# Optimization experiments

Measured on AMD Instinct MI355X. Metric: run time of the kernel, lower is better.

The kernel has to match this reference:

```python
import jax, jax.numpy as jnp
import numpy as np

BS, C, D = 4096, 16384, 128
POS_ALPHA, POS_DELTA = 32.0, 0.1
NEG_ALPHA, NEG_DELTA = 32.0, -0.1


def _normalize(x):
    # F.normalize(x, dim=1)
    return x / jnp.linalg.norm(x, axis=1, keepdims=True)


def _masked_lse(sims, mask, axis, use_max):
    """Faithful port of Criterion.masked_logsumexp (returns per-entry lse and the
    nonzero-entry mask that torch uses to filter before the final mean)."""
    m = sims * mask
    if use_max:
        ref = jnp.max(m, axis=axis, keepdims=True)
    else:
        ref = jnp.min(m, axis=axis, keepdims=True)
    ref = jax.lax.stop_gradient(ref)  # torch: ref_v.detach()
    # torch: nz_entries = max + min of (sims*mask); keep where nonzero
    nz = (jnp.max(m, axis=axis) + jnp.min(m, axis=axis)) != 0
    s = jnp.sum(jnp.exp(sims - ref) * mask, axis=axis)
    lse = jnp.log(jnp.where(nz, s, 1.0)) + jnp.squeeze(ref, axis=axis)
    return lse, nz


def setup_inputs() -> dict:
    key = jax.random.key(0)
    k1, k2, k3 = jax.random.split(key, 3)
    batch = jax.random.normal(k1, (BS, D), dtype=jnp.float32)
    # proxies = randn/proxy_div, init_dev=0 so no max-shift
    proxies = jax.random.normal(k2, (C, D), dtype=jnp.float32) / 8.0
    labels = jax.random.randint(k3, (BS,), 0, C)
    return {"batch": batch, "proxies": proxies, "labels": labels}


def reference(batch, proxies, labels):
    batch = _normalize(batch)          # [BS, D]
    proxies = _normalize(proxies)      # [C, D]

    pos_sims = batch @ proxies[labels].T   # [BS, BS] cosine sims to positive proxies
    sims = batch @ proxies.T               # [BS, C]

    same = (labels[:, None] == labels[None, :]).astype(batch.dtype)              # [BS, BS]
    diff = (labels[:, None] != jnp.arange(C)[None, :]).astype(batch.dtype)       # [BS, C]

    w_pos = -POS_ALPHA * (pos_sims - POS_DELTA)
    w_neg = NEG_ALPHA * (sims - NEG_DELTA)

    # mode='anchor' -> dim=0; cosine -> max=False for pos, max=True for neg
    pos_lse, pos_nz = _masked_lse(w_pos, same, axis=0, use_max=False)
    neg_lse, neg_nz = _masked_lse(w_neg, diff, axis=0, use_max=True)

    # nca_clean=False -> softplus
    pos_s = jax.nn.softplus(pos_lse)
    neg_s = jax.nn.softplus(neg_lse)

    # torch takes mean only over nz entries
    pos_mean = jnp.sum(jnp.where(pos_nz, pos_s, 0.0)) / jnp.maximum(jnp.sum(pos_nz), 1).astype(batch.dtype)
    neg_mean = jnp.sum(jnp.where(neg_nz, neg_s, 0.0)) / jnp.maximum(jnp.sum(neg_nz), 1).astype(batch.dtype)
    return pos_mean + neg_mean
```

## Files before the change

kernel.cpp:

```cpp
#include <hip/hip_runtime.h>
#include <math.h>

#define BS 4096
#define C_CLS 16384
#define D 128
#define NS 16
#define KE 46.16624130844683f
#define POS_C 4.616624130844683f
#define LN2 0.69314718055994531f
#define CORR_BLOCKS 1024
#define NEG_BLOCKS 1024

typedef __attribute__((ext_vector_type(8))) short short8;
typedef __attribute__((ext_vector_type(4))) float f32x4;

__device__ inline float bf2f(unsigned short h) {
    return __uint_as_float(((unsigned)h) << 16);
}
__device__ inline unsigned short f2bf(float f) {
    unsigned u = __float_as_uint(f);
    u += 0x7FFF + ((u >> 16) & 1);
    return (unsigned short)(u >> 16);
}
__device__ inline float fast_exp2(float x) {
#if __has_builtin(__builtin_amdgcn_exp2f)
    return __builtin_amdgcn_exp2f(x);
#else
    return exp2f(x);
#endif
}
__device__ inline float softplus(float x) {
    return fmaxf(x, 0.0f) + log1pf(__expf(-fabsf(x)));
}
__device__ inline void gload16(const void* g, void* l) {
    __builtin_amdgcn_global_load_lds((const __attribute__((address_space(1))) void*)g,
                                     (__attribute__((address_space(3))) void*)l, 16, 0, 0);
}
__device__ inline unsigned fenc(float f) {
    unsigned u = __float_as_uint(f);
    return (u & 0x80000000u) ? ~u : (u | 0x80000000u);
}
__device__ inline float fdec(unsigned k) {
    return (k & 0x80000000u) ? __uint_as_float(k ^ 0x80000000u) : __uint_as_float(~k);
}

__global__ __launch_bounds__(256) void normalize_all(const float* __restrict__ batch,
                                                     const float* __restrict__ proxies,
                                                     short* __restrict__ bbf,
                                                     short* __restrict__ pbf,
                                                     float* __restrict__ acc,
                                                     float* __restrict__ negSub,
                                                     float* __restrict__ posSum,
                                                     float* __restrict__ posCnt,
                                                     unsigned* __restrict__ posMaxK,
                                                     unsigned* __restrict__ posMinK,
                                                     int* __restrict__ counter) {
    const int w = threadIdx.x >> 6, lane = threadIdx.x & 63;
    const int row = blockIdx.x * 4 + w;
    const bool isb = row < BS;
    const float* src = isb ? batch : proxies;
    short* dst = isb ? bbf : pbf;
    const int r = isb ? row : row - BS;
    const float sc = isb ? 1.0f : KE;

    float2 v = ((const float2*)(src + (size_t)r * D))[lane];
    float ss = v.x * v.x + v.y * v.y;
#pragma unroll
    for (int off = 32; off; off >>= 1) ss += __shfl_xor(ss, off);
    float inv = rsqrtf(ss) * sc;
    ushort2 o;
    o.x = f2bf(v.x * inv);
    o.y = f2bf(v.y * inv);
    ((ushort2*)(dst + (size_t)r * D))[lane] = o;

    const int bid = blockIdx.x, t = bid * 256 + threadIdx.x;
    if (bid < 64) negSub[t] = 0.0f;
    else if (bid < 128) posSum[t - 64 * 256] = 0.0f;
    else if (bid < 192) posCnt[t - 128 * 256] = 0.0f;
    else if (bid < 256) posMaxK[t - 192 * 256] = 0u;
    else if (bid < 320) posMinK[t - 256 * 256] = 0xFFFFFFFFu;
    if (bid == 0) {
        if (threadIdx.x < 4) acc[threadIdx.x] = 0.0f;
        if (threadIdx.x == 4) *counter = 0;
    }
}

__global__ __launch_bounds__(256, 4) void mm_all(const short* __restrict__ pbf,
                                                 const short* __restrict__ bbf,
                                                 const int* __restrict__ labels,
                                                 float* __restrict__ S,
                                                 float* __restrict__ negSub,
                                                 float* __restrict__ posSum,
                                                 float* __restrict__ posCnt,
                                                 unsigned* __restrict__ posMaxK,
                                                 unsigned* __restrict__ posMinK) {
    __shared__ short8 frag[2][16 * 64];

    const int bid = blockIdx.x;
    const int tid = threadIdx.x;
    const int w = tid >> 6, lane = tid & 63, l16 = lane & 15, g = lane >> 4;

    if (bid < CORR_BLOCKS) {
        const int i = bid * 4 + w;
        const int lab = labels[i];
        ushort2 av = ((const ushort2*)(bbf + (size_t)i * D))[lane];
        ushort2 pv = ((const ushort2*)(pbf + (size_t)lab * D))[lane];
        float d = bf2f(av.x) * bf2f(pv.x) + bf2f(av.y) * bf2f(pv.y);
#pragma unroll
        for (int off = 32; off; off >>= 1) d += __shfl_xor(d, off);
        if (lane == 0) {
            atomicAdd(&negSub[lab], fast_exp2(d));
            atomicAdd(&posSum[lab], fast_exp2(POS_C - d));
            atomicAdd(&posCnt[lab], 1.0f);
            float wv = fmaf(d, -LN2, 3.2f);
            unsigned k = fenc(wv);
            atomicMax(&posMaxK[lab], k);
            atomicMin(&posMinK[lab], k);
        }
    } else {
        const int n = bid - CORR_BLOCKS;
        const int pg = (n & 7) * 8 + ((n >> 3) & 7);
        const int sp = n >> 6;
        const int wbase = pg * 256 + w * 64;

        short8 a[4][4];
#pragma unroll
        for (int pt = 0; pt < 4; pt++)
#pragma unroll
            for (int kk = 0; kk < 4; kk++)
                a[pt][kk] = *(const short8*)(pbf + (size_t)(wbase + pt * 16 + l16) * D + kk * 32 + g * 8);

        float s[4][4];
#pragma unroll
        for (int pt = 0; pt < 4; pt++)
#pragma unroll
            for (int r = 0; r < 4; r++) s[pt][r] = 0.0f;

        const int ibeg = sp * (BS / NS);
        const short* srcbase = bbf + (size_t)(ibeg + w * 16 + l16) * D + g * 8;

#pragma unroll
        for (int kk = 0; kk < 4; kk++)
            gload16(srcbase + kk * 32, &frag[0][(w * 4 + kk) * 64]);
        asm volatile("s_waitcnt vmcnt(0)" ::: "memory");
        __syncthreads();

        for (int rnd = 0; rnd < 4; rnd++) {
            const int cur = rnd & 1;
            if (rnd < 3) {
                const short* sn = srcbase + (size_t)(rnd + 1) * 64 * D;
#pragma unroll
                for (int kk = 0; kk < 4; kk++)
                    gload16(sn + kk * 32, &frag[cur ^ 1][(w * 4 + kk) * 64]);
            }
            __builtin_amdgcn_s_setprio(1);
#pragma unroll
            for (int bt = 0; bt < 4; bt++) {
                short8 b[4];
#pragma unroll
                for (int kk = 0; kk < 4; kk++) b[kk] = frag[cur][(bt * 4 + kk) * 64 + lane];
#pragma unroll
                for (int pt = 0; pt < 4; pt++) {
                    f32x4 acc = {0.0f, 0.0f, 0.0f, 0.0f};
#pragma unroll
                    for (int kk = 0; kk < 4; kk++)
                        acc = __builtin_amdgcn_mfma_f32_16x16x32_bf16(a[pt][kk], b[kk], acc, 0, 0, 0);
#pragma unroll
                    for (int r = 0; r < 4; r++) s[pt][r] += fast_exp2(acc[r]);
                }
            }
            __builtin_amdgcn_s_setprio(0);
            asm volatile("s_waitcnt vmcnt(0)" ::: "memory");
            __syncthreads();
        }

#pragma unroll
        for (int off = 1; off < 16; off <<= 1)
#pragma unroll
            for (int pt = 0; pt < 4; pt++)
#pragma unroll
                for (int r = 0; r < 4; r++) s[pt][r] += __shfl_xor(s[pt][r], off);

        if (l16 == 0) {
#pragma unroll
            for (int pt = 0; pt < 4; pt++)
#pragma unroll
                for (int r = 0; r < 4; r++) {
                    int row = wbase + pt * 16 + g * 4 + r;
                    S[(size_t)sp * C_CLS + row] = s[pt][r];
                }
        }
    }
}

__global__ __launch_bounds__(256) void final_reduce(const float* __restrict__ S,
                                                    const float* __restrict__ negSub,
                                                    const int* __restrict__ labels,
                                                    const float* __restrict__ posSum,
                                                    const float* __restrict__ posCnt,
                                                    const unsigned* __restrict__ posMaxK,
                                                    const unsigned* __restrict__ posMinK,
                                                    float* __restrict__ acc,
                                                    int* __restrict__ counter,
                                                    float* __restrict__ out) {
    const int n = blockIdx.x * 256 + threadIdx.x;
    float add = 0.0f, cnt = 0.0f;
    int slot;
    if (n < C_CLS) {
        slot = 2;
        float s = 0.0f;
#pragma unroll
        for (int p = 0; p < NS; p++) s += S[(size_t)p * C_CLS + n];
        s = fmaxf(s - negSub[n], 1e-30f);
        add = softplus(logf(s) + 3.2f);
        cnt = 1.0f;
    } else {
        slot = 0;
        const int j = n - C_CLS;
        const int lab = labels[j];
        float s = posSum[lab], c = posCnt[lab];
        float mxw = fdec(posMaxK[lab]), mnw = fdec(posMinK[lab]);
        float maxm = (c < (float)BS) ? fmaxf(mxw, 0.0f) : mxw;
        float minm = (c < (float)BS) ? fminf(mnw, 0.0f) : mnw;
        bool nz = (maxm + minm) != 0.0f;
        if (nz) {
            add = softplus(logf(s));
            cnt = 1.0f;
        }
    }
#pragma unroll
    for (int off = 32; off; off >>= 1) {
        add += __shfl_xor(add, off);
        cnt += __shfl_xor(cnt, off);
    }
    if ((threadIdx.x & 63) == 0) {
        atomicAdd(&acc[slot], add);
        atomicAdd(&acc[slot + 1], cnt);
    }

    __shared__ int amLast;
    __threadfence();
    if (threadIdx.x == 0) amLast = (atomicAdd(counter, 1) == (int)gridDim.x - 1);
    __syncthreads();
    if (amLast && threadIdx.x == 0) {
        __threadfence();
        out[0] = acc[0] / fmaxf(acc[1], 1.0f) + acc[2] / fmaxf(acc[3], 1.0f);
    }
}

extern "C" void kernel_launch(void* const* d_in, const int* in_sizes, int n_in,
                              void* d_out, int out_size, void* d_ws, size_t ws_size,
                              hipStream_t stream) {
    const float* batch = (const float*)d_in[0];
    const float* proxies = (const float*)d_in[1];
    const int* labels = (const int*)d_in[2];
    float* out = (float*)d_out;

    char* ws = (char*)d_ws;
    float* acc = (float*)ws;
    int* counter = (int*)(ws + 64);
    short* bbf = (short*)(ws + 256);
    short* pbf = (short*)(ws + 256 + (size_t)BS * D * 2);
    char* p = ws + 256 + (size_t)(BS + C_CLS) * D * 2;
    float* negS = (float*)p;       p += (size_t)C_CLS * NS * 4;
    float* negSub = (float*)p;     p += (size_t)C_CLS * 4;
    float* posSum = (float*)p;     p += (size_t)C_CLS * 4;
    float* posCnt = (float*)p;     p += (size_t)C_CLS * 4;
    unsigned* posMaxK = (unsigned*)p; p += (size_t)C_CLS * 4;
    unsigned* posMinK = (unsigned*)p;

    normalize_all<<<(BS + C_CLS) / 4, 256, 0, stream>>>(batch, proxies, bbf, pbf, acc,
                                                        negSub, posSum, posCnt, posMaxK,
                                                        posMinK, counter);
    mm_all<<<CORR_BLOCKS + NEG_BLOCKS, 256, 0, stream>>>(pbf, bbf, labels, negS, negSub,
                                                         posSum, posCnt, posMaxK, posMinK);
    final_reduce<<<(C_CLS + BS) / 256, 256, 0, stream>>>(negS, negSub, labels, posSum,
                                                         posCnt, posMaxK, posMinK,
                                                         acc, counter, out);
}
```

Measured before the change: 50.87 us.

## Halve batch splits and use triple-buffered LDS pipeline with partial waits

```diff
diff --git a/kernel.cpp b/kernel.cpp
--- a/kernel.cpp
+++ b/kernel.cpp
@@ -4,12 +4,13 @@
 #define BS 4096
 #define C_CLS 16384
 #define D 128
-#define NS 16
+#define NS 8
+#define NR 8
 #define KE 46.16624130844683f
 #define POS_C 4.616624130844683f
 #define LN2 0.69314718055994531f
 #define CORR_BLOCKS 1024
-#define NEG_BLOCKS 1024
+#define NEG_BLOCKS 512
 
 typedef __attribute__((ext_vector_type(8))) short short8;
 typedef __attribute__((ext_vector_type(4))) float f32x4;
@@ -94,7 +95,7 @@
                                                  float* __restrict__ posCnt,
                                                  unsigned* __restrict__ posMaxK,
                                                  unsigned* __restrict__ posMinK) {
-    __shared__ short8 frag[2][16 * 64];
+    __shared__ short8 frag[3][16 * 64];
 
     const int bid = blockIdx.x;
     const int tid = threadIdx.x;
@@ -117,79 +118,87 @@
             atomicMax(&posMaxK[lab], k);
             atomicMin(&posMinK[lab], k);
         }
-    } else {
-        const int n = bid - CORR_BLOCKS;
-        const int pg = (n & 7) * 8 + ((n >> 3) & 7);
-        const int sp = n >> 6;
-        const int wbase = pg * 256 + w * 64;
-
-        short8 a[4][4];
+        return;
+    }
+
+    const int n = bid - CORR_BLOCKS;
+    const int pg = (n & 7) * 8 + ((n >> 3) & 7);
+    const int sp = n >> 6;
+    const int wbase = pg * 256 + w * 64;
+
+    short8 a[4][4];
+#pragma unroll
+    for (int pt = 0; pt < 4; pt++)
+#pragma unroll
+        for (int kk = 0; kk < 4; kk++)
+            a[pt][kk] = *(const short8*)(pbf + (size_t)(wbase + pt * 16 + l16) * D + kk * 32 + g * 8);
+    asm volatile("" ::: "memory");
+
+    const int ibeg = sp * (BS / NS);
+    const short* srcbase = bbf + (size_t)(ibeg + w * 16 + l16) * D + g * 8;
+
+#define STAGE(rr)                                                            \
+    {                                                                        \
+        const short* sn_ = srcbase + (size_t)(rr) * 64 * D;                  \
+        _Pragma("unroll") for (int kk = 0; kk < 4; kk++)                     \
+            gload16(sn_ + kk * 32, &frag[(rr) % 3][(w * 4 + kk) * 64]);      \
+    }
+
+    STAGE(0)
+    STAGE(1)
+
+    float s[4][4];
+#pragma unroll
+    for (int pt = 0; pt < 4; pt++)
+#pragma unroll
+        for (int r = 0; r < 4; r++) s[pt][r] = 0.0f;
+
+#pragma unroll
+    for (int rnd = 0; rnd < NR; rnd++) {
+        if (rnd < NR - 1)
+            asm volatile("s_waitcnt vmcnt(4)" ::: "memory");
+        else
+            asm volatile("s_waitcnt vmcnt(0)" ::: "memory");
+        __builtin_amdgcn_s_barrier();
+
+        const short8* fb = &frag[rnd % 3][0];
+        __builtin_amdgcn_s_setprio(1);
+#pragma unroll
+        for (int bt = 0; bt < 4; bt++) {
+            short8 b[4];
+#pragma unroll
+            for (int kk = 0; kk < 4; kk++) b[kk] = fb[(bt * 4 + kk) * 64 + lane];
+#pragma unroll
+            for (int pt = 0; pt < 4; pt++) {
+                f32x4 acc = {0.0f, 0.0f, 0.0f, 0.0f};
+#pragma unroll
+                for (int kk = 0; kk < 4; kk++)
+                    acc = __builtin_amdgcn_mfma_f32_16x16x32_bf16(a[pt][kk], b[kk], acc, 0, 0, 0);
+#pragma unroll
+                for (int r = 0; r < 4; r++) s[pt][r] += fast_exp2(acc[r]);
+            }
+        }
+        __builtin_amdgcn_s_setprio(0);
+
+        if (rnd + 2 < NR) STAGE(rnd + 2)
+    }
+#undef STAGE
+
+#pragma unroll
+    for (int off = 1; off < 16; off <<= 1)
 #pragma unroll
         for (int pt = 0; pt < 4; pt++)
 #pragma unroll
-            for (int kk = 0; kk < 4; kk++)
-                a[pt][kk] = *(const short8*)(pbf + (size_t)(wbase + pt * 16 + l16) * D + kk * 32 + g * 8);
-
-        float s[4][4];
+            for (int r = 0; r < 4; r++) s[pt][r] += __shfl_xor(s[pt][r], off);
+
+    if (l16 == 0) {
 #pragma unroll
         for (int pt = 0; pt < 4; pt++)
 #pragma unroll
-            for (int r = 0; r < 4; r++) s[pt][r] = 0.0f;
-
-        const int ibeg = sp * (BS / NS);
-        const short* srcbase = bbf + (size_t)(ibeg + w * 16 + l16) * D + g * 8;
-
-#pragma unroll
-        for (int kk = 0; kk < 4; kk++)
-            gload16(srcbase + kk * 32, &frag[0][(w * 4 + kk) * 64]);
-        asm volatile("s_waitcnt vmcnt(0)" ::: "memory");
-        __syncthreads();
-
-        for (int rnd = 0; rnd < 4; rnd++) {
-            const int cur = rnd & 1;
-            if (rnd < 3) {
-                const short* sn = srcbase + (size_t)(rnd + 1) * 64 * D;
-#pragma unroll
-                for (int kk = 0; kk < 4; kk++)
-                    gload16(sn + kk * 32, &frag[cur ^ 1][(w * 4 + kk) * 64]);
+            for (int r = 0; r < 4; r++) {
+                int row = wbase + pt * 16 + g * 4 + r;
+                S[(size_t)sp * C_CLS + row] = s[pt][r];
             }
-            __builtin_amdgcn_s_setprio(1);
-#pragma unroll
-            for (int bt = 0; bt < 4; bt++) {
-                short8 b[4];
-#pragma unroll
-                for (int kk = 0; kk < 4; kk++) b[kk] = frag[cur][(bt * 4 + kk) * 64 + lane];
-#pragma unroll
-                for (int pt = 0; pt < 4; pt++) {
-                    f32x4 acc = {0.0f, 0.0f, 0.0f, 0.0f};
-#pragma unroll
-                    for (int kk = 0; kk < 4; kk++)
-                        acc = __builtin_amdgcn_mfma_f32_16x16x32_bf16(a[pt][kk], b[kk], acc, 0, 0, 0);
-#pragma unroll
-                    for (int r = 0; r < 4; r++) s[pt][r] += fast_exp2(acc[r]);
-                }
-            }
-            __builtin_amdgcn_s_setprio(0);
-            asm volatile("s_waitcnt vmcnt(0)" ::: "memory");
-            __syncthreads();
-        }
-
-#pragma unroll
-        for (int off = 1; off < 16; off <<= 1)
-#pragma unroll
-            for (int pt = 0; pt < 4; pt++)
-#pragma unroll
-                for (int r = 0; r < 4; r++) s[pt][r] += __shfl_xor(s[pt][r], off);
-
-        if (l16 == 0) {
-#pragma unroll
-            for (int pt = 0; pt < 4; pt++)
-#pragma unroll
-                for (int r = 0; r < 4; r++) {
-                    int row = wbase + pt * 16 + g * 4 + r;
-                    S[(size_t)sp * C_CLS + row] = s[pt][r];
-                }
-        }
     }
 }
 
```

After: 53.47 us. 1.05x slower.
